# Kernel optimization log

Hardware: AMD Instinct MI355X
Metric: run time of the kernel (lower is better)

Reference implementation:

```python
import jax, jax.numpy as jnp
import numpy as np

K = 20          # neighbors
M = 8           # weight-bank size per layer
EPS = 1e-5      # BatchNorm eps


def _bn(x, axes):
    # training-mode BatchNorm at init (gamma=1, beta=0), biased variance like torch
    mu = x.mean(axes, keepdims=True)
    var = x.var(axes, keepdims=True)
    return (x - mu) * jax.lax.rsqrt(var + EPS)


def _gather(feat, idx):
    # feat [B,N,C], idx [B,N,K] -> neighbor features [B,N,K,C]
    return jax.vmap(lambda f, i: f[i])(feat, idx)


def _knn_idx(x):
    # x [B,C,N]; pairwise_distance = -||xi||^2 + 2 xi.xj - ||xj||^2 (neg sq dist)
    sq = jnp.sum(x * x, axis=1)                      # [B,N]
    inner = jnp.einsum('bcn,bcm->bnm', x, x)          # [B,N,N]
    pd = 2.0 * inner - sq[:, :, None] - sq[:, None, :]
    return jax.lax.top_k(pd, K)[1]                    # [B,N,K]


def _scorenet(xyz, w1, w2, b):
    # xyz [B,N,K,6]; 1x1 Conv2d == channel-last matmul; BN2d over (B,N,K)
    h = jax.nn.relu(_bn(xyz @ w1, (0, 1, 2)))         # [B,N,K,16]
    s = h @ w2 + b                                    # [B,N,K,M]
    return jax.nn.softmax(s, axis=-1) + 0.5           # softmax over m, bias=0.5


def _paconv(feat, idx, ker, score):
    # feat [B,N,C]; ker [2C, M*O]; score [B,N,K,M]
    # torch: point = concat(x,x) @ ker -> [B,N,M,O]; center = x @ ker[:C]
    # assemble_dgcnn (assign_score_withk, aggregate='sum'):
    #   out[b,n,o] = sum_{k,m} score[b,n,k,m] * (point[b, idx[b,n,k], m, o] - center[b, n, m, o])
    C = feat.shape[-1]
    k3 = ker.reshape(2 * C, M, -1)
    Wa, Wb = k3[:C], k3[C:]                           # point uses Wa+Wb (x repeated); center uses Wa
    nf = _gather(feat, idx)                           # [B,N,K,C]
    T = jnp.einsum('bnkm,bnkc->bnmc', score, nf)      # score-weighted neighbor feats
    out = jnp.einsum('bnmc,cmo->bno', T, Wa + Wb)
    out = out - jnp.einsum('bnm,bnc,cmo->bno', score.sum(2), feat, Wa)
    return jax.nn.relu(_bn(out, (0, 1)))              # BN1d over (B,N), channel-last


def setup_inputs() -> dict:
    key = jax.random.key(0)
    ks = jax.random.split(key, 18)
    B, N = 32, 1024
    dims = [(3, 64), (64, 64), (64, 128), (128, 256)]
    d = {"x": jax.random.normal(ks[0], (B, 3, N), dtype=jnp.float32)}
    for i, (ci, co) in enumerate(dims):
        scale = (2.0 / (2 * ci)) ** 0.5  # kaiming_normal over fan_in=2*ci
        d[f"mat{i+1}"] = jax.random.normal(ks[1 + i], (2 * ci, M * co), dtype=jnp.float32) * scale
        d[f"sn{i+1}_w1"] = jax.random.normal(ks[5 + i], (6, 16), dtype=jnp.float32) * 0.4
        d[f"sn{i+1}_w2"] = jax.random.normal(ks[9 + i], (16, M), dtype=jnp.float32) * 0.25
        d[f"sn{i+1}_b"] = jnp.zeros((M,), dtype=jnp.float32)
    d["conv5_w"] = jax.random.normal(ks[13], (512, 1024), dtype=jnp.float32) * 0.04
    d["lin1_w"] = jax.random.normal(ks[14], (2048, 512), dtype=jnp.float32) * 0.02
    d["lin2_w"] = jax.random.normal(ks[15], (512, 256), dtype=jnp.float32) * 0.04
    d["lin3_w"] = jax.random.normal(ks[16], (256, 40), dtype=jnp.float32) * 0.06
    d["lin3_b"] = jnp.zeros((40,), dtype=jnp.float32)
    return d


def reference(x, mat1, mat2, mat3, mat4,
              sn1_w1, sn1_w2, sn1_b, sn2_w1, sn2_w2, sn2_b,
              sn3_w1, sn3_w2, sn3_b, sn4_w1, sn4_w2, sn4_b,
              conv5_w, lin1_w, lin2_w, lin3_w, lin3_b):
    idx = _knn_idx(x)                                  # [B,N,K]
    xT = jnp.swapaxes(x, 1, 2)                         # [B,N,3]
    nx = _gather(xT, idx)                              # [B,N,K,3]
    xyz = jnp.concatenate([nx - xT[:, :, None, :], nx], axis=-1)  # [B,N,K,6]

    p1 = _paconv(xT, idx, mat1, _scorenet(xyz, sn1_w1, sn1_w2, sn1_b))  # [B,N,64]
    p2 = _paconv(p1, idx, mat2, _scorenet(xyz, sn2_w1, sn2_w2, sn2_b))  # [B,N,64]
    p3 = _paconv(p2, idx, mat3, _scorenet(xyz, sn3_w1, sn3_w2, sn3_b))  # [B,N,128]
    p4 = _paconv(p3, idx, mat4, _scorenet(xyz, sn4_w1, sn4_w2, sn4_b))  # [B,N,256]

    p = jnp.concatenate([p1, p2, p3, p4], axis=-1)     # [B,N,512]
    p = jax.nn.relu(_bn(p @ conv5_w, (0, 1)))          # [B,N,1024]
    g = jnp.concatenate([p.max(axis=1), p.mean(axis=1)], axis=-1)  # [B,2048]
    h = jax.nn.relu(_bn(g @ lin1_w, (0,)))             # [B,512] (dropout = identity)
    h = jax.nn.relu(_bn(h @ lin2_w, (0,)))             # [B,256]
    return h @ lin3_w + lin3_b                         # [B,40]
```

## Files before the change

kernel.cpp:

```cpp
#include <hip/hip_runtime.h>
#include <cstdint>
#include <cstddef>

static constexpr int Bc  = 32;
static constexpr int Nc  = 1024;
static constexpr int Kc  = 20;
static constexpr int Mc  = 8;
static constexpr int BNc = Bc * Nc;
static constexpr int BNKc = BNc * Kc;

typedef __attribute__((ext_vector_type(4))) float f32x4;
typedef _Float16 f16x8 __attribute__((ext_vector_type(8)));

__device__ inline short f2h(float v) { _Float16 h = (_Float16)v; return __builtin_bit_cast(short, h); }
__device__ inline float h2f(short s) { return (float)__builtin_bit_cast(_Float16, s); }

__global__ void zero_kernel(float* p, int n) {
  int gid = blockIdx.x * blockDim.x + threadIdx.x;
  if (gid < n) p[gid] = 0.f;
}

__global__ __launch_bounds__(256) void knn_kernel(const float* __restrict__ x,
                                                  int* __restrict__ idxout) {
  int wv = threadIdx.x >> 6;
  int bn = blockIdx.x * 4 + wv;
  int b = bn >> 10, n = bn & (Nc - 1);
  int lane = threadIdx.x & 63;
  const float* xb = x + (size_t)b * 3 * Nc;
  float cx = xb[n], cy = xb[Nc + n], cz = xb[2 * Nc + n];
  float sqc = cx * cx + cy * cy + cz * cz;
  float d[16];
#pragma unroll
  for (int j = 0; j < 16; j++) {
    int m2 = j * 64 + lane;
    float xm = xb[m2], ym = xb[Nc + m2], zm = xb[2 * Nc + m2];
    d[j] = 2.f * (cx * xm + cy * ym + cz * zm) - sqc - (xm * xm + ym * ym + zm * zm);
  }
  int* out = idxout + (size_t)bn * Kc;
  for (int kk = 0; kk < Kc; kk++) {
    float bd = d[0]; int bj = 0;
#pragma unroll
    for (int j = 1; j < 16; j++)
      if (d[j] > bd) { bd = d[j]; bj = j; }
    int bm = bj * 64 + lane;
#pragma unroll
    for (int off = 32; off; off >>= 1) {
      float od = __shfl_down(bd, off);
      int   om = __shfl_down(bm, off);
      if (od > bd || (od == bd && om < bm)) { bd = od; bm = om; }
    }
    bm = __shfl(bm, 0);
    if (lane == 0) out[kk] = bm;
    int bmj = bm >> 6;
    bool mine = (bm & 63) == lane;
#pragma unroll
    for (int j = 0; j < 16; j++)
      if (mine && j == bmj) d[j] = -3e38f;
  }
}

__global__ __launch_bounds__(256) void xt_kernel(const float* __restrict__ x,
                                                 float* __restrict__ xT) {
  int gid = blockIdx.x * blockDim.x + threadIdx.x;
  int c = gid % 3;
  int bn = gid / 3;
  int b = bn >> 10, n = bn & (Nc - 1);
  xT[gid] = x[((size_t)b * 3 + c) * Nc + n];
}

__device__ inline void xyz_at(const float* __restrict__ xT, const int* __restrict__ idx,
                              int e, float v[6]) {
  int bn = e / Kc;
  int b = bn >> 10;
  int nb = idx[e];
  const float* pc = xT + (size_t)bn * 3;
  const float* pn = xT + ((size_t)(b << 10) + nb) * 3;
#pragma unroll
  for (int c = 0; c < 3; c++) { float nv = pn[c]; v[c] = nv - pc[c]; v[3 + c] = nv; }
}

__global__ __launch_bounds__(256) void xyz_stats_kernel(const float* __restrict__ xT,
                                                        const int* __restrict__ idx,
                                                        float* __restrict__ accum) {
  __shared__ float sPart[4 * 42];
  int tid = threadIdx.x;
  int gid = blockIdx.x * 256 + tid;
  float a[42];
#pragma unroll
  for (int t = 0; t < 42; t++) a[t] = 0.f;
  for (int i = 0; i < 8; i++) {
    float v[6];
    xyz_at(xT, idx, gid + i * 81920, v);
#pragma unroll
    for (int c = 0; c < 6; c++) a[c] += v[c];
    int t = 6;
#pragma unroll
    for (int c = 0; c < 6; c++)
#pragma unroll
      for (int d = 0; d < 6; d++) a[t++] += v[c] * v[d];
  }
  int lane = tid & 63, wid = tid >> 6;
#pragma unroll
  for (int t = 0; t < 42; t++) {
    float v = a[t];
#pragma unroll
    for (int off = 32; off; off >>= 1) v += __shfl_down(v, off);
    if (lane == 0) sPart[wid * 42 + t] = v;
  }
  __syncthreads();
  if (tid < 42) {
    float s = sPart[tid] + sPart[42 + tid] + sPart[84 + tid] + sPart[126 + tid];
    atomicAdd(&accum[tid], s);
  }
}

__global__ void snstats_kernel(const float* __restrict__ accum,
                               const float* __restrict__ w1a, const float* __restrict__ w1b,
                               const float* __restrict__ w1c, const float* __restrict__ w1d,
                               float* __restrict__ snstats) {
  int t = threadIdx.x;
  int l = t >> 4, j = t & 15;
  const float* w1 = (l == 0) ? w1a : (l == 1) ? w1b : (l == 2) ? w1c : w1d;
  const float invc = 1.f / (float)BNKc;
  float wj[6];
  float mu = 0.f;
#pragma unroll
  for (int c = 0; c < 6; c++) { wj[c] = w1[c * 16 + j]; mu += accum[c] * invc * wj[c]; }
  float e2 = 0.f;
#pragma unroll
  for (int c = 0; c < 6; c++)
#pragma unroll
    for (int d = 0; d < 6; d++) e2 += wj[c] * wj[d] * (accum[6 + c * 6 + d] * invc);
  float var = e2 - mu * mu;
  snstats[t * 2] = mu;
  snstats[t * 2 + 1] = rsqrtf(var + 1e-5f);
}

__global__ __launch_bounds__(256) void score_kernel(const float* __restrict__ xT,
                                                    const int* __restrict__ idx,
                                                    const float* __restrict__ w1,
                                                    const float* __restrict__ w2,
                                                    const float* __restrict__ bias,
                                                    const float* __restrict__ snst,
                                                    float* __restrict__ score) {
  __shared__ float sW1[96], sW2[128], sB[8], sMu[16], sRs[16];
  int tid = threadIdx.x;
  if (tid < 96) sW1[tid] = w1[tid];
  else if (tid < 224) sW2[tid - 96] = w2[tid - 96];
  else if (tid < 232) sB[tid - 224] = bias[tid - 224];
  else if (tid < 248) { sMu[tid - 232] = snst[(tid - 232) * 2]; sRs[tid - 232] = snst[(tid - 232) * 2 + 1]; }
  __syncthreads();
  int e = blockIdx.x * 256 + tid;
  float v[6];
  xyz_at(xT, idx, e, v);
  float h[16];
#pragma unroll
  for (int j = 0; j < 16; j++) {
    float a = 0.f;
#pragma unroll
    for (int c = 0; c < 6; c++) a += v[c] * sW1[c * 16 + j];
    a = (a - sMu[j]) * sRs[j];
    h[j] = a > 0.f ? a : 0.f;
  }
  float s[8];
  float mx = -3e38f;
#pragma unroll
  for (int m = 0; m < 8; m++) {
    float a = sB[m];
#pragma unroll
    for (int j = 0; j < 16; j++) a += h[j] * sW2[j * 8 + m];
    s[m] = a;
    mx = fmaxf(mx, a);
  }
  float sum = 0.f;
#pragma unroll
  for (int m = 0; m < 8; m++) { s[m] = expf(s[m] - mx); sum += s[m]; }
  float inv = 1.f / sum;
#pragma unroll
  for (int m = 0; m < 8; m++) score[(size_t)e * 8 + m] = s[m] * inv + 0.5f;
}

template <int C, int Co, int MH>
__global__ __launch_bounds__(256) void paconv_kernel(
    const float* __restrict__ feat, int fstride,
    const float* __restrict__ ker,
    const float* __restrict__ score,
    const int* __restrict__ idx,
    float* __restrict__ outp, int ostride) {
  constexpr int PT = 8;
  constexpr int MS = Mc / MH;
  __shared__ float sX[PT][2 * MH * C];
  __shared__ float sSc[PT * Kc * Mc];
  __shared__ int sIdx[PT * Kc];
  __shared__ float sFc[PT][C];
  __shared__ float sSum[PT][Mc];

  int tid = threadIdx.x;
  int pbase = blockIdx.x * PT;
  int bN = pbase & ~(Nc - 1);

  for (int e = tid; e < PT * Kc; e += 256) sIdx[e] = idx[(size_t)pbase * Kc + e];
  for (int e = tid; e < PT * Kc * Mc; e += 256) sSc[e] = score[(size_t)pbase * Kc * Mc + e];
  for (int e = tid; e < PT * C; e += 256) {
    int p = e / C, c = e - p * C;
    sFc[p][c] = feat[(size_t)(pbase + p) * fstride + c];
  }
  __syncthreads();
  for (int e = tid; e < PT * Mc; e += 256) {
    int p = e >> 3, m = e & 7;
    float s = 0.f;
#pragma unroll
    for (int k = 0; k < Kc; k++) s += sSc[p * Kc * Mc + k * Mc + m];
    sSum[p][m] = s;
  }
  __syncthreads();

  constexpr int OG = Co;
  constexpr int PG = 256 / OG;
  constexpr int PPT = PT / PG;
  int o = tid % OG;
  int pg = tid / OG;
  float acc[PPT];
#pragma unroll
  for (int i = 0; i < PPT; i++) acc[i] = 0.f;

  for (int ms = 0; ms < MS; ms++) {
    int mb = ms * MH;
    for (int e = tid; e < PT * C; e += 256) {
      int p = e / C, c = e - p * C;
      float t[MH];
#pragma unroll
      for (int mm = 0; mm < MH; mm++) t[mm] = 0.f;
      const float* sc = &sSc[p * Kc * Mc + mb];
      for (int k = 0; k < Kc; k++) {
        float v = feat[(size_t)(bN + sIdx[p * Kc + k]) * fstride + c];
#pragma unroll
        for (int mm = 0; mm < MH; mm++) t[mm] += sc[k * Mc + mm] * v;
      }
      float fc = sFc[p][c];
#pragma unroll
      for (int mm = 0; mm < MH; mm++) {
        sX[p][mm * C + c] = t[mm] - sSum[p][mb + mm] * fc;
        sX[p][MH * C + mm * C + c] = t[mm];
      }
    }
    __syncthreads();
#pragma unroll
    for (int mm = 0; mm < MH; mm++) {
      int m = mb + mm;
      const float* kerm = ker + (size_t)m * Co + o;
      for (int c = 0; c < C; c++) {
        float wA = kerm[(size_t)c * (Mc * Co)];
        float wB = kerm[(size_t)(C + c) * (Mc * Co)];
        int r = mm * C + c;
#pragma unroll
        for (int i = 0; i < PPT; i++) {
          int p = pg * PPT + i;
          acc[i] += sX[p][r] * wA;
          acc[i] += sX[p][MH * C + r] * wB;
        }
      }
    }
    __syncthreads();
  }

#pragma unroll
  for (int i = 0; i < PPT; i++) {
    int p = pg * PPT + i;
    outp[(size_t)(pbase + p) * ostride + o] = acc[i];
  }
}

template <int C>
__global__ __launch_bounds__(256) void gather_kernel(
    const short* __restrict__ pb, int coff,
    const float* __restrict__ score,
    const int* __restrict__ idx,
    short* __restrict__ T, short* __restrict__ sumb) {
  constexpr int PT = 256 / C;
  constexpr int KH = Mc * C;
  __shared__ float sSc[PT][Kc][Mc];
  __shared__ int   sIdx[PT][Kc];
  int tid = threadIdx.x;
  int pbase = blockIdx.x * PT;
  int bbase = pbase & ~(Nc - 1);
  for (int e = tid; e < PT * Kc * Mc; e += 256) (&sSc[0][0][0])[e] = score[(size_t)pbase * Kc * Mc + e];
  for (int e = tid; e < PT * Kc; e += 256) (&sIdx[0][0])[e] = idx[(size_t)pbase * Kc + e];
  __syncthreads();
  if (tid < PT * Mc) {
    int p = tid >> 3, m = tid & 7;
    float s = 0.f;
#pragma unroll
    for (int k = 0; k < Kc; k++) s += sSc[p][k][m];
    sumb[(size_t)(pbase + p) * 8 + m] = f2h(s);
  }
  int p = tid / C, c = tid - p * C;
  float t[Mc];
#pragma unroll
  for (int m = 0; m < Mc; m++) t[m] = 0.f;
  for (int k = 0; k < Kc; k++) {
    float v = h2f(pb[(size_t)(bbase + sIdx[p][k]) * 512 + coff + c]);
#pragma unroll
    for (int m = 0; m < Mc; m++) t[m] += sSc[p][k][m] * v;
  }
  short* rowp = T + (size_t)(pbase + p) * KH;
#pragma unroll
  for (int m = 0; m < Mc; m++) rowp[m * C + c] = f2h(t[m]);
}

__global__ __launch_bounds__(256) void kerconv_r1_kernel(const float* __restrict__ ker,
                                                         short* __restrict__ Bt,
                                                         int C, int Co, int total) {
  int gid = blockIdx.x * 256 + threadIdx.x;
  if (gid >= total) return;
  int KH = Mc * C;
  int K2 = 2 * KH;
  int o = gid / K2, r = gid - o * K2;
  float v;
  if (r < KH) {
    int m = r / C, c = r - m * C;
    v = ker[(size_t)c * (Mc * Co) + m * Co + o] + ker[(size_t)(C + c) * (Mc * Co) + m * Co + o];
  } else {
    int r2 = r - KH;
    int m = r2 / C, c = r2 - m * C;
    v = -ker[(size_t)c * (Mc * Co) + m * Co + o];
  }
  Bt[gid] = f2h(v);
}

__global__ __launch_bounds__(256) void w5conv_kernel(const float* __restrict__ W,
                                                     short* __restrict__ Wt) {
  int gid = blockIdx.x * 256 + threadIdx.x;
  int o = gid >> 9, k = gid & 511;
  Wt[gid] = f2h(W[(size_t)k * 1024 + o]);
}

template <int BM, int BN, bool OUT_HALF>
__global__ __launch_bounds__(256) void gemm_kernel(
    const short* __restrict__ A,
    const short* __restrict__ Bt,
    int K,
    void* __restrict__ Cout, int ldc) {
  constexpr int BK = 64;
  constexpr int FN = BN / 32;
  constexpr int FMW = BM / 32;
  __shared__ short sA[BM * BK];
  __shared__ short sB[BN * BK];
  int tid = threadIdx.x;
  int lane = tid & 63, wv = tid >> 6;
  int wrow = (wv & 1) * (BM / 2);
  int wcol = (wv >> 1) * (BN / 2);
  int bm0 = blockIdx.x * BM;
  int bn0 = blockIdx.y * BN;
  int r15 = lane & 15, quad = lane >> 4;
  int swz = r15 & 7;

  f32x4 acc[FMW][FN];
#pragma unroll
  for (int fm = 0; fm < FMW; fm++)
#pragma unroll
    for (int fn = 0; fn < FN; fn++) acc[fm][fn] = (f32x4){0.f, 0.f, 0.f, 0.f};

  for (int k0 = 0; k0 < K; k0 += BK) {
#pragma unroll
    for (int i = 0; i < (BM * BK / 8) / 256; i++) {
      int cb = i * 256 + wv * 64;
      int chunk = cb + lane;
      int row = chunk >> 3, kc = (chunk & 7) ^ (row & 7);
      const short* g = A + (size_t)(bm0 + row) * K + k0 + kc * 8;
      __builtin_amdgcn_global_load_lds((const __attribute__((address_space(1))) void*)g,
                                       (__attribute__((address_space(3))) void*)&sA[cb * 8],
                                       16, 0, 0);
    }
#pragma unroll
    for (int i = 0; i < (BN * BK / 8) / 256; i++) {
      int cb = i * 256 + wv * 64;
      int chunk = cb + lane;
      int row = chunk >> 3, kc = (chunk & 7) ^ (row & 7);
      const short* g = Bt + (size_t)(bn0 + row) * K + k0 + kc * 8;
      __builtin_amdgcn_global_load_lds((const __attribute__((address_space(1))) void*)g,
                                       (__attribute__((address_space(3))) void*)&sB[cb * 8],
                                       16, 0, 0);
    }
    __syncthreads();
#pragma unroll
    for (int kk = 0; kk < BK; kk += 32) {
      f16x8 af[FMW], bf[FN];
      int ccol = (kk >> 3) + quad;
#pragma unroll
      for (int fm = 0; fm < FMW; fm++)
        af[fm] = *(const f16x8*)&sA[(wrow + fm * 16 + r15) * BK + ((ccol ^ swz) * 8)];
#pragma unroll
      for (int fn = 0; fn < FN; fn++)
        bf[fn] = *(const f16x8*)&sB[(wcol + fn * 16 + r15) * BK + ((ccol ^ swz) * 8)];
#pragma unroll
      for (int fm = 0; fm < FMW; fm++)
#pragma unroll
        for (int fn = 0; fn < FN; fn++)
          acc[fm][fn] = __builtin_amdgcn_mfma_f32_16x16x32_f16(af[fm], bf[fn], acc[fm][fn], 0, 0, 0);
    }
    __syncthreads();
  }

#pragma unroll
  for (int fn = 0; fn < FN; fn++) {
    int col = bn0 + wcol + fn * 16 + r15;
#pragma unroll
    for (int fm = 0; fm < FMW; fm++) {
      int rowb = bm0 + wrow + fm * 16 + quad * 4;
#pragma unroll
      for (int r = 0; r < 4; r++) {
        float v = acc[fm][fn][r];
        if constexpr (OUT_HALF) ((short*)Cout)[(size_t)(rowb + r) * ldc + col] = f2h(v);
        else                    ((float*)Cout)[(size_t)(rowb + r) * ldc + col] = v;
      }
    }
  }
}

template <int BM, int BN, int C>
__global__ __launch_bounds__(256) void gemm_r1_kernel(
    const short* __restrict__ T,
    const short* __restrict__ Bt,
    const short* __restrict__ pb, int coff,
    const short* __restrict__ sumb,
    short* __restrict__ Cout, int ldc) {
  constexpr int BK = 64;
  constexpr int KH = Mc * C;
  constexpr int K2 = 2 * KH;
  constexpr int FN = BN / 32;
  constexpr int FMW = BM / 32;
  __shared__ short sA[BM * BK];
  __shared__ short sB[BN * BK];
  __shared__ short sFc[BM * C];
  __shared__ short sSm[BM * 8];
  int tid = threadIdx.x;
  int lane = tid & 63, wv = tid >> 6;
  int wrow = (wv & 1) * (BM / 2);
  int wcol = (wv >> 1) * (BN / 2);
  int bm0 = blockIdx.x * BM;
  int bn0 = blockIdx.y * BN;
  int r15 = lane & 15, quad = lane >> 4;
  int swz = r15 & 7;

  for (int e = tid; e < BM * C; e += 256) {
    int p = e / C, c = e - p * C;
    sFc[e] = pb[(size_t)(bm0 + p) * 512 + coff + c];
  }
  for (int e = tid; e < BM * 8; e += 256) sSm[e] = sumb[(size_t)bm0 * 8 + e];

  f32x4 acc[FMW][FN];
#pragma unroll
  for (int fm = 0; fm < FMW; fm++)
#pragma unroll
    for (int fn = 0; fn < FN; fn++) acc[fm][fn] = (f32x4){0.f, 0.f, 0.f, 0.f};
  __syncthreads();

  for (int k0 = 0; k0 < K2; k0 += BK) {
    if (k0 < KH) {
#pragma unroll
      for (int i = 0; i < (BM * BK / 8) / 256; i++) {
        int cb = i * 256 + wv * 64;
        int chunk = cb + lane;
        int row = chunk >> 3, kc = (chunk & 7) ^ (row & 7);
        const short* g = T + (size_t)(bm0 + row) * KH + k0 + kc * 8;
        __builtin_amdgcn_global_load_lds((const __attribute__((address_space(1))) void*)g,
                                         (__attribute__((address_space(3))) void*)&sA[cb * 8],
                                         16, 0, 0);
      }
    } else {
#pragma unroll
      for (int i = 0; i < (BM * BK / 8) / 256; i++) {
        int cb = i * 256 + wv * 64;
        int chunk = cb + lane;
        int row = chunk >> 3, kc = (chunk & 7) ^ (row & 7);
        int kb = (k0 - KH) + kc * 8;
        int m = kb / C, c = kb - m * C;
        _Float16 sm = __builtin_bit_cast(_Float16, sSm[row * 8 + m]);
        f16x8 fcv = *(const f16x8*)&sFc[row * C + c];
        f16x8 val;
#pragma unroll
        for (int j = 0; j < 8; j++) val[j] = sm * fcv[j];
        *(f16x8*)&sA[chunk * 8] = val;
      }
    }
#pragma unroll
    for (int i = 0; i < (BN * BK / 8) / 256; i++) {
      int cb = i * 256 + wv * 64;
      int chunk = cb + lane;
      int row = chunk >> 3, kc = (chunk & 7) ^ (row & 7);
      const short* g = Bt + (size_t)(bn0 + row) * K2 + k0 + kc * 8;
      __builtin_amdgcn_global_load_lds((const __attribute__((address_space(1))) void*)g,
                                       (__attribute__((address_space(3))) void*)&sB[cb * 8],
                                       16, 0, 0);
    }
    __syncthreads();
#pragma unroll
    for (int kk = 0; kk < BK; kk += 32) {
      f16x8 af[FMW], bf[FN];
      int ccol = (kk >> 3) + quad;
#pragma unroll
      for (int fm = 0; fm < FMW; fm++)
        af[fm] = *(const f16x8*)&sA[(wrow + fm * 16 + r15) * BK + ((ccol ^ swz) * 8)];
#pragma unroll
      for (int fn = 0; fn < FN; fn++)
        bf[fn] = *(const f16x8*)&sB[(wcol + fn * 16 + r15) * BK + ((ccol ^ swz) * 8)];
#pragma unroll
      for (int fm = 0; fm < FMW; fm++)
#pragma unroll
        for (int fn = 0; fn < FN; fn++)
          acc[fm][fn] = __builtin_amdgcn_mfma_f32_16x16x32_f16(af[fm], bf[fn], acc[fm][fn], 0, 0, 0);
    }
    __syncthreads();
  }

#pragma unroll
  for (int fn = 0; fn < FN; fn++) {
    int col = bn0 + wcol + fn * 16 + r15;
#pragma unroll
    for (int fm = 0; fm < FMW; fm++) {
      int rowb = bm0 + wrow + fm * 16 + quad * 4;
#pragma unroll
      for (int r = 0; r < 4; r++)
        Cout[(size_t)(rowb + r) * ldc + col] = f2h(acc[fm][fn][r]);
    }
  }
}

template <bool IS_HALF>
__global__ __launch_bounds__(256) void bnstats_kernel(const void* __restrict__ pre,
                                                      int Co,
                                                      float* __restrict__ bnslots) {
  __shared__ float sS[4][64], sQ[4][64];
  int tid = threadIdx.x;
  int c = tid & 63, tg = tid >> 6;
  int ch = blockIdx.x * 64 + c;
  int row0 = blockIdx.y * 1024 + tg * 256;
  float s = 0.f, q = 0.f;
  if constexpr (IS_HALF) {
    const short* p = (const short*)pre + (size_t)row0 * Co + ch;
#pragma unroll 4
    for (int r = 0; r < 256; r++) {
      float v = h2f(p[(size_t)r * Co]);
      s += v; q += v * v;
    }
  } else {
    const float* p = (const float*)pre + (size_t)row0 * Co + ch;
#pragma unroll 4
    for (int r = 0; r < 256; r++) {
      float v = p[(size_t)r * Co];
      s += v; q += v * v;
    }
  }
  sS[tg][c] = s; sQ[tg][c] = q;
  __syncthreads();
  if (tid < 64) {
    float ts = sS[0][tid] + sS[1][tid] + sS[2][tid] + sS[3][tid];
    float tq = sQ[0][tid] + sQ[1][tid] + sQ[2][tid] + sQ[3][tid];
    int chh = blockIdx.x * 64 + tid;
    bnslots[(chh * 32 + blockIdx.y) * 2 + 0] = ts;
    bnslots[(chh * 32 + blockIdx.y) * 2 + 1] = tq;
  }
}

__global__ void bnfinalize_kernel(const float* __restrict__ slots,
                                  float* __restrict__ bnmr, int Co) {
  int ch = blockIdx.x * blockDim.x + threadIdx.x;
  if (ch >= Co) return;
  float s = 0.f, q = 0.f;
#pragma unroll 4
  for (int i = 0; i < 32; i++) { s += slots[(ch * 32 + i) * 2]; q += slots[(ch * 32 + i) * 2 + 1]; }
  float mu = s / (float)BNc;
  float var = q / (float)BNc - mu * mu;
  bnmr[ch * 2] = mu;
  bnmr[ch * 2 + 1] = rsqrtf(var + 1e-5f);
}

__global__ __launch_bounds__(256) void bnapply_kernel(const float* __restrict__ pre,
                                                      int Co, const float* __restrict__ bnmr,
                                                      short* __restrict__ pb, int coff) {
  int gid = blockIdx.x * 256 + threadIdx.x;
  int row = gid / Co, ch = gid - row * Co;
  float mu = bnmr[ch * 2], rs = bnmr[ch * 2 + 1];
  float v = (pre[gid] - mu) * rs;
  pb[(size_t)row * 512 + coff + ch] = f2h(v > 0.f ? v : 0.f);
}

__global__ __launch_bounds__(256) void bnapply16_kernel(const short* __restrict__ pre,
                                                        int Co, const float* __restrict__ bnmr,
                                                        short* __restrict__ pb, int coff) {
  int gid = blockIdx.x * 256 + threadIdx.x;
  int row = gid / Co, ch = gid - row * Co;
  float mu = bnmr[ch * 2], rs = bnmr[ch * 2 + 1];
  float v = (h2f(pre[gid]) - mu) * rs;
  pb[(size_t)row * 512 + coff + ch] = f2h(v > 0.f ? v : 0.f);
}

__global__ __launch_bounds__(512) void g2_kernel(const short* __restrict__ pre,
                                                 const float* __restrict__ bnmr,
                                                 float* __restrict__ g) {
  int b = blockIdx.x, nch = blockIdx.y;
  int tid = threadIdx.x;
  int ch0 = 2 * tid;
  float mu0 = bnmr[ch0 * 2],     rs0 = bnmr[ch0 * 2 + 1];
  float mu1 = bnmr[ch0 * 2 + 2], rs1 = bnmr[ch0 * 2 + 3];
  const uint32_t* p32 = (const uint32_t*)(pre + (size_t)b * 1024 * 1024 + (size_t)nch * 128 * 1024);
  float mx0 = 0.f, mx1 = 0.f, sm0 = 0.f, sm1 = 0.f;
#pragma unroll 4
  for (int n = 0; n < 128; n++) {
    uint32_t u = p32[n * 512 + tid];
    float v0 = (h2f((short)(u & 0xffff)) - mu0) * rs0;
    float v1 = (h2f((short)(u >> 16))    - mu1) * rs1;
    v0 = v0 > 0.f ? v0 : 0.f;
    v1 = v1 > 0.f ? v1 : 0.f;
    mx0 = fmaxf(mx0, v0); mx1 = fmaxf(mx1, v1);
    sm0 += v0; sm1 += v1;
  }
  int* gi = (int*)g;
  atomicMax(&gi[b * 2048 + ch0], __float_as_int(mx0));
  atomicMax(&gi[b * 2048 + ch0 + 1], __float_as_int(mx1));
  atomicAdd(&g[b * 2048 + 1024 + ch0], sm0 * (1.f / 1024.f));
  atomicAdd(&g[b * 2048 + 1024 + ch0 + 1], sm1 * (1.f / 1024.f));
}

__global__ __launch_bounds__(256) void linsplit_kernel(const float* __restrict__ A,
                                                       const float* __restrict__ W,
                                                       float* __restrict__ out,
                                                       int Kdim, int Cols, int kchunk) {
  int j = blockIdx.x * 256 + threadIdx.x;
  if (j >= Cols) return;
  int b = blockIdx.y;
  int k0 = blockIdx.z * kchunk;
  const float* a = A + (size_t)b * Kdim + k0;
  const float* w = W + (size_t)k0 * Cols + j;
  float acc = 0.f;
#pragma unroll 4
  for (int i = 0; i < kchunk; i++) acc += a[i] * w[(size_t)i * Cols];
  atomicAdd(&out[b * Cols + j], acc);
}

__global__ __launch_bounds__(256) void biasinit_kernel(const float* __restrict__ bias,
                                                       float* __restrict__ out, int Cols, int n) {
  int gid = blockIdx.x * 256 + threadIdx.x;
  if (gid < n) out[gid] = bias[gid % Cols];
}

__global__ __launch_bounds__(256) void lin_bn_kernel(float* __restrict__ X, int Cols) {
  int j = blockIdx.x * 256 + threadIdx.x;
  if (j >= Cols) return;
  float s = 0.f, q = 0.f;
#pragma unroll
  for (int b = 0; b < 32; b++) { float v = X[b * Cols + j]; s += v; q += v * v; }
  float mu = s * (1.f / 32.f);
  float var = q * (1.f / 32.f) - mu * mu;
  float rs = rsqrtf(var + 1e-5f);
#pragma unroll
  for (int b = 0; b < 32; b++) {
    float v = (X[b * Cols + j] - mu) * rs;
    X[b * Cols + j] = v > 0.f ? v : 0.f;
  }
}

extern "C" void kernel_launch(void* const* d_in, const int* in_sizes, int n_in,
                              void* d_out, int out_size, void* d_ws, size_t ws_size,
                              hipStream_t stream) {
  (void)in_sizes; (void)n_in; (void)out_size; (void)ws_size;
  const float* x      = (const float*)d_in[0];
  const float* mat1   = (const float*)d_in[1];
  const float* sn1_w1 = (const float*)d_in[2];
  const float* sn1_w2 = (const float*)d_in[3];
  const float* sn1_b  = (const float*)d_in[4];
  const float* mat2   = (const float*)d_in[5];
  const float* sn2_w1 = (const float*)d_in[6];
  const float* sn2_w2 = (const float*)d_in[7];
  const float* sn2_b  = (const float*)d_in[8];
  const float* mat3   = (const float*)d_in[9];
  const float* sn3_w1 = (const float*)d_in[10];
  const float* sn3_w2 = (const float*)d_in[11];
  const float* sn3_b  = (const float*)d_in[12];
  const float* mat4   = (const float*)d_in[13];
  const float* sn4_w1 = (const float*)d_in[14];
  const float* sn4_w2 = (const float*)d_in[15];
  const float* sn4_b  = (const float*)d_in[16];
  const float* conv5w = (const float*)d_in[17];
  const float* lin1w  = (const float*)d_in[18];
  const float* lin2w  = (const float*)d_in[19];
  const float* lin3w  = (const float*)d_in[20];
  const float* lin3b  = (const float*)d_in[21];
  float* out = (float*)d_out;

  char* ws = (char*)d_ws;
  size_t cur = 0;
  auto alloc = [&](size_t bytes) {
    size_t r = cur;
    cur += (bytes + 1023) & ~(size_t)1023;
    return r;
  };
  size_t off_idx   = alloc((size_t)BNKc * 4);
  size_t off_xT    = alloc((size_t)BNc * 3 * 4);
  size_t off_st    = alloc((size_t)157888 * 4);
  size_t off_sum   = alloc((size_t)BNc * 8 * 2);
  size_t off_score = alloc((size_t)BNKc * 8 * 4);
  size_t off_pre   = alloc((size_t)BNc * 256 * 4);
  size_t off_pb    = alloc((size_t)BNc * 512 * 2);
  size_t off_kb    = alloc((size_t)1048576);
  size_t off_TU    = alloc((size_t)BNc * 1024 * 2);

  int*   idx   = (int*)(ws + off_idx);
  float* xT    = (float*)(ws + off_xT);
  float* stats = (float*)(ws + off_st);
  short* sumb  = (short*)(ws + off_sum);
  float* score = (float*)(ws + off_score);
  float* pre   = (float*)(ws + off_pre);
  short* pre16 = (short*)(ws + off_pre);
  short* pb    = (short*)(ws + off_pb);
  short* kb    = (short*)(ws + off_kb);
  short* T     = (short*)(ws + off_TU);
  short* pre5  = (short*)(ws + off_TU);

  float* xyzacc  = stats;
  float* snstats = stats + 64;
  float* bnslots = stats + 192;
  float* bnmr    = stats + 65728;
  float* g       = stats + 67776;
  float* h1      = stats + 133312;
  float* h2      = stats + 149696;

  zero_kernel<<<1, 64, 0, stream>>>(xyzacc, 64);
  knn_kernel<<<BNc / 4, 256, 0, stream>>>(x, idx);
  xt_kernel<<<BNc * 3 / 256, 256, 0, stream>>>(x, xT);
  xyz_stats_kernel<<<320, 256, 0, stream>>>(xT, idx, xyzacc);
  snstats_kernel<<<1, 64, 0, stream>>>(xyzacc, sn1_w1, sn2_w1, sn3_w1, sn4_w1, snstats);

  score_kernel<<<BNKc / 256, 256, 0, stream>>>(xT, idx, sn1_w1, sn1_w2, sn1_b, snstats + 0, score);
  paconv_kernel<3, 64, 8><<<BNc / 8, 256, 0, stream>>>(xT, 3, mat1, score, idx, pre, 64);
  bnstats_kernel<false><<<dim3(1, 32), 256, 0, stream>>>(pre, 64, bnslots);
  bnfinalize_kernel<<<1, 64, 0, stream>>>(bnslots, bnmr, 64);
  bnapply_kernel<<<BNc * 64 / 256, 256, 0, stream>>>(pre, 64, bnmr, pb, 0);

  score_kernel<<<BNKc / 256, 256, 0, stream>>>(xT, idx, sn2_w1, sn2_w2, sn2_b, snstats + 32, score);
  gather_kernel<64><<<BNc / 4, 256, 0, stream>>>(pb, 0, score, idx, T, sumb);
  kerconv_r1_kernel<<<64 * 1024 / 256, 256, 0, stream>>>(mat2, kb, 64, 64, 64 * 1024);
  gemm_r1_kernel<64, 64, 64><<<dim3(512, 1), 256, 0, stream>>>(T, kb, pb, 0, sumb, pre16, 64);
  bnstats_kernel<true><<<dim3(1, 32), 256, 0, stream>>>(pre16, 64, bnslots);
  bnfinalize_kernel<<<1, 64, 0, stream>>>(bnslots, bnmr, 64);
  bnapply16_kernel<<<BNc * 64 / 256, 256, 0, stream>>>(pre16, 64, bnmr, pb, 64);

  score_kernel<<<BNKc / 256, 256, 0, stream>>>(xT, idx, sn3_w1, sn3_w2, sn3_b, snstats + 64, score);
  gather_kernel<64><<<BNc / 4, 256, 0, stream>>>(pb, 64, score, idx, T, sumb);
  kerconv_r1_kernel<<<128 * 1024 / 256, 256, 0, stream>>>(mat3, kb, 64, 128, 128 * 1024);
  gemm_r1_kernel<64, 128, 64><<<dim3(512, 1), 256, 0, stream>>>(T, kb, pb, 64, sumb, pre16, 128);
  bnstats_kernel<true><<<dim3(2, 32), 256, 0, stream>>>(pre16, 128, bnslots);
  bnfinalize_kernel<<<1, 128, 0, stream>>>(bnslots, bnmr, 128);
  bnapply16_kernel<<<BNc * 128 / 256, 256, 0, stream>>>(pre16, 128, bnmr, pb, 128);

  score_kernel<<<BNKc / 256, 256, 0, stream>>>(xT, idx, sn4_w1, sn4_w2, sn4_b, snstats + 96, score);
  gather_kernel<128><<<BNc / 2, 256, 0, stream>>>(pb, 128, score, idx, T, sumb);
  kerconv_r1_kernel<<<256 * 2048 / 256, 256, 0, stream>>>(mat4, kb, 128, 256, 256 * 2048);
  gemm_r1_kernel<64, 128, 128><<<dim3(512, 2), 256, 0, stream>>>(T, kb, pb, 128, sumb, pre16, 256);
  bnstats_kernel<true><<<dim3(4, 32), 256, 0, stream>>>(pre16, 256, bnslots);
  bnfinalize_kernel<<<1, 256, 0, stream>>>(bnslots, bnmr, 256);
  bnapply16_kernel<<<BNc * 256 / 256, 256, 0, stream>>>(pre16, 256, bnmr, pb, 256);

  w5conv_kernel<<<524288 / 256, 256, 0, stream>>>(conv5w, kb);
  gemm_kernel<128, 128, true><<<dim3(256, 8), 256, 0, stream>>>(pb, kb, 512, pre5, 1024);
  bnstats_kernel<true><<<dim3(16, 32), 256, 0, stream>>>(pre5, 1024, bnslots);
  bnfinalize_kernel<<<4, 256, 0, stream>>>(bnslots, bnmr, 1024);

  zero_kernel<<<256, 256, 0, stream>>>(g, 65536);
  g2_kernel<<<dim3(32, 8), 512, 0, stream>>>(pre5, bnmr, g);

  zero_kernel<<<64, 256, 0, stream>>>(h1, 16384);
  linsplit_kernel<<<dim3(2, 32, 8), 256, 0, stream>>>(g, lin1w, h1, 2048, 512, 256);
  lin_bn_kernel<<<2, 256, 0, stream>>>(h1, 512);
  zero_kernel<<<32, 256, 0, stream>>>(h2, 8192);
  linsplit_kernel<<<dim3(1, 32, 4), 256, 0, stream>>>(h1, lin2w, h2, 512, 256, 128);
  lin_bn_kernel<<<1, 256, 0, stream>>>(h2, 256);
  biasinit_kernel<<<5, 256, 0, stream>>>(lin3b, out, 40, 1280);
  linsplit_kernel<<<dim3(1, 32, 2), 256, 0, stream>>>(h2, lin3w, out, 256, 40, 128);
}
```

Before: 813.7 us.

## Fuse four scorenet passes into one kernel with fp16 scores; batch weight conversions

Replaces four separate score_kernel launches with one score4_kernel. It gathers each point's xyz neighborhood once, evaluates all four scorenets, and writes the scores as fp16 instead of fp32. The four per-layer weight conversion kernels become a single kerconv_all_kernel launched up front, writing into a larger shared weight buffer. This removes three redundant gathers and launches and halves score traffic. In exchange it needs four times the score storage and stores scores at reduced precision.

```diff
diff --git a/kernel.cpp b/kernel.cpp
--- a/kernel.cpp
+++ b/kernel.cpp
@@ -136,55 +136,63 @@
   snstats[t * 2 + 1] = rsqrtf(var + 1e-5f);
 }
 
-__global__ __launch_bounds__(256) void score_kernel(const float* __restrict__ xT,
-                                                    const int* __restrict__ idx,
-                                                    const float* __restrict__ w1,
-                                                    const float* __restrict__ w2,
-                                                    const float* __restrict__ bias,
-                                                    const float* __restrict__ snst,
-                                                    float* __restrict__ score) {
-  __shared__ float sW1[96], sW2[128], sB[8], sMu[16], sRs[16];
+__global__ __launch_bounds__(256) void score4_kernel(
+    const float* __restrict__ xT, const int* __restrict__ idx,
+    const float* __restrict__ w1a, const float* __restrict__ w2a, const float* __restrict__ b1,
+    const float* __restrict__ w1b, const float* __restrict__ w2b, const float* __restrict__ b2,
+    const float* __restrict__ w1c, const float* __restrict__ w2c, const float* __restrict__ b3,
+    const float* __restrict__ w1d, const float* __restrict__ w2d, const float* __restrict__ b4,
+    const float* __restrict__ snst, short* __restrict__ score4) {
+  __shared__ float sW1[4][96], sW2[4][128], sB[4][8], sMu[4][16], sRs[4][16];
   int tid = threadIdx.x;
-  if (tid < 96) sW1[tid] = w1[tid];
-  else if (tid < 224) sW2[tid - 96] = w2[tid - 96];
-  else if (tid < 232) sB[tid - 224] = bias[tid - 224];
-  else if (tid < 248) { sMu[tid - 232] = snst[(tid - 232) * 2]; sRs[tid - 232] = snst[(tid - 232) * 2 + 1]; }
+  if (tid < 96) { sW1[0][tid] = w1a[tid]; sW1[1][tid] = w1b[tid]; sW1[2][tid] = w1c[tid]; sW1[3][tid] = w1d[tid]; }
+  else if (tid < 224) { int t = tid - 96; sW2[0][t] = w2a[t]; sW2[1][t] = w2b[t]; sW2[2][t] = w2c[t]; sW2[3][t] = w2d[t]; }
+  else if (tid < 232) { int t = tid - 224; sB[0][t] = b1[t]; sB[1][t] = b2[t]; sB[2][t] = b3[t]; sB[3][t] = b4[t]; }
+  else if (tid < 248) {
+    int t = tid - 232;
+#pragma unroll
+    for (int l = 0; l < 4; l++) { sMu[l][t] = snst[(l * 16 + t) * 2]; sRs[l][t] = snst[(l * 16 + t) * 2 + 1]; }
+  }
   __syncthreads();
   int e = blockIdx.x * 256 + tid;
   float v[6];
   xyz_at(xT, idx, e, v);
-  float h[16];
-#pragma unroll
-  for (int j = 0; j < 16; j++) {
-    float a = 0.f;
-#pragma unroll
-    for (int c = 0; c < 6; c++) a += v[c] * sW1[c * 16 + j];
-    a = (a - sMu[j]) * sRs[j];
-    h[j] = a > 0.f ? a : 0.f;
-  }
-  float s[8];
-  float mx = -3e38f;
-#pragma unroll
-  for (int m = 0; m < 8; m++) {
-    float a = sB[m];
-#pragma unroll
-    for (int j = 0; j < 16; j++) a += h[j] * sW2[j * 8 + m];
-    s[m] = a;
-    mx = fmaxf(mx, a);
-  }
-  float sum = 0.f;
-#pragma unroll
-  for (int m = 0; m < 8; m++) { s[m] = expf(s[m] - mx); sum += s[m]; }
-  float inv = 1.f / sum;
-#pragma unroll
-  for (int m = 0; m < 8; m++) score[(size_t)e * 8 + m] = s[m] * inv + 0.5f;
+#pragma unroll
+  for (int l = 0; l < 4; l++) {
+    float h[16];
+#pragma unroll
+    for (int j = 0; j < 16; j++) {
+      float a = 0.f;
+#pragma unroll
+      for (int c = 0; c < 6; c++) a += v[c] * sW1[l][c * 16 + j];
+      a = (a - sMu[l][j]) * sRs[l][j];
+      h[j] = a > 0.f ? a : 0.f;
+    }
+    float s[8];
+    float mx = -3e38f;
+#pragma unroll
+    for (int m = 0; m < 8; m++) {
+      float a = sB[l][m];
+#pragma unroll
+      for (int j = 0; j < 16; j++) a += h[j] * sW2[l][j * 8 + m];
+      s[m] = a;
+      mx = fmaxf(mx, a);
+    }
+    float sum = 0.f;
+#pragma unroll
+    for (int m = 0; m < 8; m++) { s[m] = expf(s[m] - mx); sum += s[m]; }
+    float inv = 1.f / sum;
+    short* op = score4 + (size_t)l * BNKc * 8 + (size_t)e * 8;
+#pragma unroll
+    for (int m = 0; m < 8; m++) op[m] = f2h(s[m] * inv + 0.5f);
+  }
 }
 
 template <int C, int Co, int MH>
 __global__ __launch_bounds__(256) void paconv_kernel(
     const float* __restrict__ feat, int fstride,
     const float* __restrict__ ker,
-    const float* __restrict__ score,
+    const short* __restrict__ score,
     const int* __restrict__ idx,
     float* __restrict__ outp, int ostride) {
   constexpr int PT = 8;
@@ -200,7 +208,7 @@
   int bN = pbase & ~(Nc - 1);
 
   for (int e = tid; e < PT * Kc; e += 256) sIdx[e] = idx[(size_t)pbase * Kc + e];
-  for (int e = tid; e < PT * Kc * Mc; e += 256) sSc[e] = score[(size_t)pbase * Kc * Mc + e];
+  for (int e = tid; e < PT * Kc * Mc; e += 256) sSc[e] = h2f(score[(size_t)pbase * Kc * Mc + e]);
   for (int e = tid; e < PT * C; e += 256) {
     int p = e / C, c = e - p * C;
     sFc[p][c] = feat[(size_t)(pbase + p) * fstride + c];
@@ -274,7 +282,7 @@
 template <int C>
 __global__ __launch_bounds__(256) void gather_kernel(
     const short* __restrict__ pb, int coff,
-    const float* __restrict__ score,
+    const short* __restrict__ score,
     const int* __restrict__ idx,
     short* __restrict__ T, short* __restrict__ sumb) {
   constexpr int PT = 256 / C;
@@ -284,7 +292,7 @@
   int tid = threadIdx.x;
   int pbase = blockIdx.x * PT;
   int bbase = pbase & ~(Nc - 1);
-  for (int e = tid; e < PT * Kc * Mc; e += 256) (&sSc[0][0][0])[e] = score[(size_t)pbase * Kc * Mc + e];
+  for (int e = tid; e < PT * Kc * Mc; e += 256) (&sSc[0][0][0])[e] = h2f(score[(size_t)pbase * Kc * Mc + e]);
   for (int e = tid; e < PT * Kc; e += 256) (&sIdx[0][0])[e] = idx[(size_t)pbase * Kc + e];
   __syncthreads();
   if (tid < PT * Mc) {
@@ -308,14 +316,23 @@
   for (int m = 0; m < Mc; m++) rowp[m * C + c] = f2h(t[m]);
 }
 
-__global__ __launch_bounds__(256) void kerconv_r1_kernel(const float* __restrict__ ker,
-                                                         short* __restrict__ Bt,
-                                                         int C, int Co, int total) {
+__global__ __launch_bounds__(256) void kerconv_all_kernel(
+    const float* __restrict__ m2, const float* __restrict__ m3,
+    const float* __restrict__ m4, const float* __restrict__ w5,
+    short* __restrict__ kb) {
   int gid = blockIdx.x * 256 + threadIdx.x;
-  if (gid >= total) return;
-  int KH = Mc * C;
-  int K2 = 2 * KH;
-  int o = gid / K2, r = gid - o * K2;
+  const float* ker; short* dst; int C, Co, g;
+  if (gid < 65536)       { ker = m2; dst = kb;          C = 64;  Co = 64;  g = gid; }
+  else if (gid < 196608) { ker = m3; dst = kb + 65536;  C = 64;  Co = 128; g = gid - 65536; }
+  else if (gid < 720896) { ker = m4; dst = kb + 196608; C = 128; Co = 256; g = gid - 196608; }
+  else {
+    int g5 = gid - 720896;
+    int o = g5 >> 9, k = g5 & 511;
+    kb[720896 + g5] = f2h(w5[(size_t)k * 1024 + o]);
+    return;
+  }
+  int KH = Mc * C, K2 = 2 * KH;
+  int o = g / K2, r = g - o * K2;
   float v;
   if (r < KH) {
     int m = r / C, c = r - m * C;
@@ -325,14 +342,7 @@
     int m = r2 / C, c = r2 - m * C;
     v = -ker[(size_t)c * (Mc * Co) + m * Co + o];
   }
-  Bt[gid] = f2h(v);
-}
-
-__global__ __launch_bounds__(256) void w5conv_kernel(const float* __restrict__ W,
-                                                     short* __restrict__ Wt) {
-  int gid = blockIdx.x * 256 + threadIdx.x;
-  int o = gid >> 9, k = gid & 511;
-  Wt[gid] = f2h(W[(size_t)k * 1024 + o]);
+  dst[g] = f2h(v);
 }
 
 template <int BM, int BN, bool OUT_HALF>
@@ -700,23 +710,23 @@
   size_t off_xT    = alloc((size_t)BNc * 3 * 4);
   size_t off_st    = alloc((size_t)157888 * 4);
   size_t off_sum   = alloc((size_t)BNc * 8 * 2);
-  size_t off_score = alloc((size_t)BNKc * 8 * 4);
+  size_t off_score = alloc((size_t)BNKc * 8 * 2 * 4);
   size_t off_pre   = alloc((size_t)BNc * 256 * 4);
   size_t off_pb    = alloc((size_t)BNc * 512 * 2);
-  size_t off_kb    = alloc((size_t)1048576);
+  size_t off_kb    = alloc((size_t)1245184 * 2);
   size_t off_TU    = alloc((size_t)BNc * 1024 * 2);
 
-  int*   idx   = (int*)(ws + off_idx);
-  float* xT    = (float*)(ws + off_xT);
-  float* stats = (float*)(ws + off_st);
-  short* sumb  = (short*)(ws + off_sum);
-  float* score = (float*)(ws + off_score);
-  float* pre   = (float*)(ws + off_pre);
-  short* pre16 = (short*)(ws + off_pre);
-  short* pb    = (short*)(ws + off_pb);
-  short* kb    = (short*)(ws + off_kb);
-  short* T     = (short*)(ws + off_TU);
-  short* pre5  = (short*)(ws + off_TU);
+  int*   idx    = (int*)(ws + off_idx);
+  float* xT     = (float*)(ws + off_xT);
+  float* stats  = (float*)(ws + off_st);
+  short* sumb   = (short*)(ws + off_sum);
+  short* score4 = (short*)(ws + off_score);
+  float* pre    = (float*)(ws + off_pre);
+  short* pre16  = (short*)(ws + off_pre);
+  short* pb     = (short*)(ws + off_pb);
+  short* kb     = (short*)(ws + off_kb);
+  short* T      = (short*)(ws + off_TU);
+  short* pre5   = (short*)(ws + off_TU);
 
   float* xyzacc  = stats;
   float* snstats = stats + 64;
@@ -732,38 +742,44 @@
   xyz_stats_kernel<<<320, 256, 0, stream>>>(xT, idx, xyzacc);
   snstats_kernel<<<1, 64, 0, stream>>>(xyzacc, sn1_w1, sn2_w1, sn3_w1, sn4_w1, snstats);
 
-  score_kernel<<<BNKc / 256, 256, 0, stream>>>(xT, idx, sn1_w1, sn1_w2, sn1_b, snstats + 0, score);
-  paconv_kernel<3, 64, 8><<<BNc / 8, 256, 0, stream>>>(xT, 3, mat1, score, idx, pre, 64);
+  score4_kernel<<<BNKc / 256, 256, 0, stream>>>(
+      xT, idx, sn1_w1, sn1_w2, sn1_b, sn2_w1, sn2_w2, sn2_b,
+      sn3_w1, sn3_w2, sn3_b, sn4_w1, sn4_w2, sn4_b, snstats, score4);
+  kerconv_all_kernel<<<4864, 256, 0, stream>>>(mat2, mat3, mat4, conv5w, kb);
+
+  short* sc1 = score4;
+  short* sc2 = score4 + (size_t)1 * BNKc * 8;
+  short* sc3 = score4 + (size_t)2 * BNKc * 8;
+  short* sc4 = score4 + (size_t)3 * BNKc * 8;
+  short* kbL2 = kb;
+  short* kbL3 = kb + 65536;
+  short* kbL4 = kb + 196608;
+  short* kbW5 = kb + 720896;
+
+  paconv_kernel<3, 64, 8><<<BNc / 8, 256, 0, stream>>>(xT, 3, mat1, sc1, idx, pre, 64);
   bnstats_kernel<false><<<dim3(1, 32), 256, 0, stream>>>(pre, 64, bnslots);
   bnfinalize_kernel<<<1, 64, 0, stream>>>(bnslots, bnmr, 64);
   bnapply_kernel<<<BNc * 64 / 256, 256, 0, stream>>>(pre, 64, bnmr, pb, 0);
 
-  score_kernel<<<BNKc / 256, 256, 0, stream>>>(xT, idx, sn2_w1, sn2_w2, sn2_b, snstats + 32, score);
-  gather_kernel<64><<<BNc / 4, 256, 0, stream>>>(pb, 0, score, idx, T, sumb);
-  kerconv_r1_kernel<<<64 * 1024 / 256, 256, 0, stream>>>(mat2, kb, 64, 64, 64 * 1024);
-  gemm_r1_kernel<64, 64, 64><<<dim3(512, 1), 256, 0, stream>>>(T, kb, pb, 0, sumb, pre16, 64);
+  gather_kernel<64><<<BNc / 4, 256, 0, stream>>>(pb, 0, sc2, idx, T, sumb);
+  gemm_r1_kernel<64, 64, 64><<<dim3(512, 1), 256, 0, stream>>>(T, kbL2, pb, 0, sumb, pre16, 64);
   bnstats_kernel<true><<<dim3(1, 32), 256, 0, stream>>>(pre16, 64, bnslots);
   bnfinalize_kernel<<<1, 64, 0, stream>>>(bnslots, bnmr, 64);
   bnapply16_kernel<<<BNc * 64 / 256, 256, 0, stream>>>(pre16, 64, bnmr, pb, 64);
 
-  score_kernel<<<BNKc / 256, 256, 0, stream>>>(xT, idx, sn3_w1, sn3_w2, sn3_b, snstats + 64, score);
-  gather_kernel<64><<<BNc / 4, 256, 0, stream>>>(pb, 64, score, idx, T, sumb);
-  kerconv_r1_kernel<<<128 * 1024 / 256, 256, 0, stream>>>(mat3, kb, 64, 128, 128 * 1024);
-  gemm_r1_kernel<64, 128, 64><<<dim3(512, 1), 256, 0, stream>>>(T, kb, pb, 64, sumb, pre16, 128);
+  gather_kernel<64><<<BNc / 4, 256, 0, stream>>>(pb, 64, sc3, idx, T, sumb);
+  gemm_r1_kernel<64, 128, 64><<<dim3(512, 1), 256, 0, stream>>>(T, kbL3, pb, 64, sumb, pre16, 128);
   bnstats_kernel<true><<<dim3(2, 32), 256, 0, stream>>>(pre16, 128, bnslots);
   bnfinalize_kernel<<<1, 128, 0, stream>>>(bnslots, bnmr, 128);
   bnapply16_kernel<<<BNc * 128 / 256, 256, 0, stream>>>(pre16, 128, bnmr, pb, 128);
 
-  score_kernel<<<BNKc / 256, 256, 0, stream>>>(xT, idx, sn4_w1, sn4_w2, sn4_b, snstats + 96, score);
-  gather_kernel<128><<<BNc / 2, 256, 0, stream>>>(pb, 128, score, idx, T, sumb);
-  kerconv_r1_kernel<<<256 * 2048 / 256, 256, 0, stream>>>(mat4, kb, 128, 256, 256 * 2048);
-  gemm_r1_kernel<64, 128, 128><<<dim3(512, 2), 256, 0, stream>>>(T, kb, pb, 128, sumb, pre16, 256);
+  gather_kernel<128><<<BNc / 2, 256, 0, stream>>>(pb, 128, sc4, idx, T, sumb);
+  gemm_r1_kernel<64, 128, 128><<<dim3(512, 2), 256, 0, stream>>>(T, kbL4, pb, 128, sumb, pre16, 256);
   bnstats_kernel<true><<<dim3(4, 32), 256, 0, stream>>>(pre16, 256, bnslots);
   bnfinalize_kernel<<<1, 256, 0, stream>>>(bnslots, bnmr, 256);
   bnapply16_kernel<<<BNc * 256 / 256, 256, 0, stream>>>(pre16, 256, bnmr, pb, 256);
 
-  w5conv_kernel<<<524288 / 256, 256, 0, stream>>>(conv5w, kb);
-  gemm_kernel<128, 128, true><<<dim3(256, 8), 256, 0, stream>>>(pb, kb, 512, pre5, 1024);
+  gemm_kernel<128, 128, true><<<dim3(256, 8), 256, 0, stream>>>(pb, kbW5, 512, pre5, 1024);
   bnstats_kernel<true><<<dim3(16, 32), 256, 0, stream>>>(pre5, 1024, bnslots);
   bnfinalize_kernel<<<4, 256, 0, stream>>>(bnslots, bnmr, 1024);
 
```

Measured after the change: 780.4 us. 1.04x faster.
